# Kernel tuning notes

Hardware: AMD Instinct MI355X
Metric: run time of the kernel (lower is better)

Reference implementation:

```python
import jax, jax.numpy as jnp
import numpy as np

LENGTH = 4000
N_PAD = 4096  # smallest power of 2 >= LENGTH


def _hadamard(n: int) -> jnp.ndarray:
    """Sylvester-construction Hadamard matrix (matches scipy.linalg.hadamard)."""
    H = np.array([[1.0]], dtype=np.float32)
    while H.shape[0] < n:
        H = np.block([[H, H], [H, -H]])
    return jnp.asarray(H, dtype=jnp.float32)


def setup_inputs() -> dict:
    key = jax.random.key(0)
    k1, k2, k3, k4 = jax.random.split(key, 4)
    x = jax.random.normal(k1, (8, 64, LENGTH), dtype=jnp.float32)          # [B, Cin, L]
    W = jax.random.normal(k2, (4, 64, 64), dtype=jnp.float32) * 0.1       # [P, Cout, Cin] (1x1 conv, no bias)
    T = jax.random.uniform(k3, (4, N_PAD), dtype=jnp.float32) / 10.0      # per-pod soft thresholds
    v = jax.random.uniform(k4, (4, N_PAD), dtype=jnp.float32)             # per-pod spectral scale
    return {"x": x, "W": W, "T": T, "v": v}


def reference(x, W, T, v):
    H = _hadamard(N_PAD)                                                  # [n, n], symmetric
    # zero-pad to power of two
    f0 = jnp.pad(x, ((0, 0), (0, 0), (0, N_PAD - LENGTH)))                # [B, Cin, n]
    # forward WHT along last axis: u @ H
    f1 = f0 @ H                                                           # [B, Cin, n]
    # per-pod: v_i * f1 -> 1x1 conv -> soft-threshold
    z = v[:, None, None, :] * f1[None]                                    # [P, B, Cin, n]
    c = jnp.einsum('poi,pbin->pbon', W, z)                                # [P, B, Cout, n]
    st = jnp.sign(c) * jax.nn.relu(jnp.abs(c) - jnp.abs(T)[:, None, None, :])
    f6 = st.sum(axis=0)                                                   # [B, Cout, n]
    # inverse WHT: u @ H / n, then crop
    y = (f6 @ H) * (1.0 / N_PAD)
    y = y[..., :LENGTH]
    return y + x  # residual
```

## Files before the change

### kernel.cpp

```cpp
#include <hip/hip_runtime.h>
#include <hip/hip_bf16.h>

#define LENGTH 4000
#define NPAD   4096
#define NB     8
#define CH     64
#define NP     4
#define NT2    32
#define BSTR   72

using ushort8 = __attribute__((ext_vector_type(8))) unsigned short;
using short8v = __attribute__((ext_vector_type(8))) short;
using f32x4   = __attribute__((ext_vector_type(4))) float;

__device__ __forceinline__ unsigned short f2bu(float f) {
    __hip_bfloat16 h = __float2bfloat16(f);
    return __builtin_bit_cast(unsigned short, h);
}
__device__ __forceinline__ float bu2f(unsigned short u) {
    __hip_bfloat16 h = __builtin_bit_cast(__hip_bfloat16, u);
    return __bfloat162float(h);
}

__device__ __forceinline__ void fwht8(float v[8]) {
    #pragma unroll
    for (int h = 1; h < 8; h <<= 1)
        #pragma unroll
        for (int j = 0; j < 8; j += 2 * h)
            #pragma unroll
            for (int k = j; k < j + h; ++k) {
                float a = v[k], b = v[k + h];
                v[k] = a + b; v[k + h] = a - b;
            }
}

#define LADR(n) ((((n) >> 3) * 9) + ((n) & 7))
#define LDSZ 4608


__global__ __launch_bounds__(512) void k_fwht_fwd(const float* __restrict__ x,
                                                  unsigned short* __restrict__ f1t,
                                                  const float* __restrict__ W,
                                                  unsigned short* __restrict__ Wb) {
    __shared__ float ldsA[LDSZ];
    __shared__ float ldsB[LDSZ];
    const int row = blockIdx.x;
    const int t = threadIdx.x;

    if (row < NP * CH && t < CH)
        Wb[row * CH + t] = f2bu(W[row * CH + t]);

    float v[8];
    if (t < 500) {
        const float* xr = x + (size_t)row * LENGTH + t * 8;
        float4 a = *(const float4*)xr, b = *(const float4*)(xr + 4);
        v[0]=a.x; v[1]=a.y; v[2]=a.z; v[3]=a.w;
        v[4]=b.x; v[5]=b.y; v[6]=b.z; v[7]=b.w;
    } else {
        #pragma unroll
        for (int j = 0; j < 8; ++j) v[j] = 0.f;
    }
    fwht8(v);

    #pragma unroll
    for (int j = 0; j < 8; ++j) ldsA[LADR(t * 8 + j)] = v[j];
    __syncthreads();
    const int s1 = (t >> 3) * 64 + (t & 7);
    #pragma unroll
    for (int j = 0; j < 8; ++j) v[j] = ldsA[LADR(s1 + j * 8)];
    fwht8(v);

    #pragma unroll
    for (int j = 0; j < 8; ++j) ldsB[LADR(s1 + j * 8)] = v[j];
    __syncthreads();
    const int s2 = (t >> 6) * 512 + ((t >> 3) & 7) * 8 + (t & 7);
    #pragma unroll
    for (int j = 0; j < 8; ++j) v[j] = ldsB[LADR(s2 + j * 64)];
    fwht8(v);

    #pragma unroll
    for (int j = 0; j < 8; ++j) ldsA[LADR(s2 + j * 64)] = v[j];
    __syncthreads();
    #pragma unroll
    for (int j = 0; j < 8; ++j) v[j] = ldsA[LADR(j * 512 + t)];
    fwht8(v);

    const int b = row >> 6, i = row & 63;
    unsigned short* fb = f1t + ((size_t)b * 128 * 64 + (size_t)i) * 32;
    #pragma unroll
    for (int j = 0; j < 8; ++j) {
        const int n = j * 512 + t;
        fb[(size_t)(n >> 5) * (64 * 32) + (n & 31)] = f2bu(v[j]);
    }
}

__global__ __launch_bounds__(256) void k_mix(const unsigned short* __restrict__ f1t,
                                             const unsigned short* __restrict__ Wb,
                                             const float* __restrict__ T,
                                             const float* __restrict__ v,
                                             unsigned short* __restrict__ f6b) {
    __shared__ unsigned short sBt[NT2 * BSTR];
    const int bid = blockIdx.x;
    const int nchunk = bid & 127;
    const int b = bid >> 7;
    const int nbase = nchunk * NT2;
    const int t = threadIdx.x;
    const int lane = t & 63;
    const int w = t >> 6;
    const int l15 = lane & 15, lq = lane >> 4;

    {
        const unsigned short* src =
            f1t + (size_t)(b * 128 + nchunk) * (64 * 32) + t * 8;
        ushort8 r = *(const ushort8*)src;
        const int i = t >> 2, n0 = (t & 3) * 8;
        #pragma unroll
        for (int j = 0; j < 8; ++j)
            sBt[(n0 + j) * BSTR + i] = r[j];
    }

    short8v afrag[NP][2];
    #pragma unroll
    for (int p = 0; p < NP; ++p)
        #pragma unroll
        for (int ks = 0; ks < 2; ++ks)
            afrag[p][ks] = *(const short8v*)(Wb +
                (size_t)(p * 64 + w * 16 + l15) * CH + ks * 32 + lq * 8);

    float vp_[2][NP], tp_[2][NP];
    #pragma unroll
    for (int nt = 0; nt < 2; ++nt) {
        const int n = nbase + nt * 16 + l15;
        #pragma unroll
        for (int p = 0; p < NP; ++p) {
            vp_[nt][p] = v[(size_t)p * NPAD + n];
            tp_[nt][p] = fabsf(T[(size_t)p * NPAD + n]);
        }
    }

    __syncthreads();

    short8v bfrag[2][2];
    #pragma unroll
    for (int nt = 0; nt < 2; ++nt)
        #pragma unroll
        for (int ks = 0; ks < 2; ++ks)
            bfrag[nt][ks] = *(const short8v*)(
                &sBt[(nt * 16 + l15) * BSTR + ks * 32 + lq * 8]);

    f32x4 acc[NP][2];
    #pragma unroll
    for (int p = 0; p < NP; ++p)
        #pragma unroll
        for (int nt = 0; nt < 2; ++nt) {
            acc[p][nt] = (f32x4){0.f, 0.f, 0.f, 0.f};
            #pragma unroll
            for (int ks = 0; ks < 2; ++ks)
                acc[p][nt] = __builtin_amdgcn_mfma_f32_16x16x32_bf16(
                    afrag[p][ks], bfrag[nt][ks], acc[p][nt], 0, 0, 0);
        }

    #pragma unroll
    for (int nt = 0; nt < 2; ++nt) {
        const int n = nbase + nt * 16 + l15;
        float outv[4] = {0.f, 0.f, 0.f, 0.f};
        #pragma unroll
        for (int p = 0; p < NP; ++p) {
            #pragma unroll
            for (int r = 0; r < 4; ++r) {
                float c = vp_[nt][p] * acc[p][nt][r];
                float a = fabsf(c) - tp_[nt][p];
                outv[r] += (a > 0.f) ? copysignf(a, c) : 0.f;
            }
        }
        #pragma unroll
        for (int r = 0; r < 4; ++r) {
            const int o = w * 16 + lq * 4 + r;
            f6b[(size_t)(b * CH + o) * NPAD + n] = f2bu(outv[r]);
        }
    }
}

__global__ __launch_bounds__(512) void k_fwht_inv(const unsigned short* __restrict__ f6b,
                                                  const float* __restrict__ x,
                                                  float* __restrict__ out) {
    __shared__ float ldsA[LDSZ];
    __shared__ float ldsB[LDSZ];
    const int row = blockIdx.x;
    const int t = threadIdx.x;

    float v[8];
    {
        const unsigned short* fr = f6b + (size_t)row * NPAD + t * 8;
        ushort8 r = *(const ushort8*)fr;
        #pragma unroll
        for (int j = 0; j < 8; ++j) v[j] = bu2f(r[j]);
    }
    fwht8(v);

    #pragma unroll
    for (int j = 0; j < 8; ++j) ldsA[LADR(t * 8 + j)] = v[j];
    __syncthreads();
    const int s1 = (t >> 3) * 64 + (t & 7);
    #pragma unroll
    for (int j = 0; j < 8; ++j) v[j] = ldsA[LADR(s1 + j * 8)];
    fwht8(v);

    #pragma unroll
    for (int j = 0; j < 8; ++j) ldsB[LADR(s1 + j * 8)] = v[j];
    __syncthreads();
    const int s2 = (t >> 6) * 512 + ((t >> 3) & 7) * 8 + (t & 7);
    #pragma unroll
    for (int j = 0; j < 8; ++j) v[j] = ldsB[LADR(s2 + j * 64)];
    fwht8(v);

    #pragma unroll
    for (int j = 0; j < 8; ++j) ldsA[LADR(s2 + j * 64)] = v[j];
    __syncthreads();
    #pragma unroll
    for (int j = 0; j < 8; ++j) v[j] = ldsA[LADR(j * 512 + t)];
    fwht8(v);

    const float scale = 1.f / NPAD;
    const float* xr = x + (size_t)row * LENGTH;
    float* orow = out + (size_t)row * LENGTH;
    #pragma unroll
    for (int j = 0; j < 8; ++j) {
        const int n = j * 512 + t;
        if (n < LENGTH) orow[n] = v[j] * scale + xr[n];
    }
}

extern "C" void kernel_launch(void* const* d_in, const int* in_sizes, int n_in,
                              void* d_out, int out_size, void* d_ws, size_t ws_size,
                              hipStream_t stream) {
    (void)in_sizes; (void)n_in; (void)out_size; (void)ws_size;
    const float* x = (const float*)d_in[0];
    const float* W = (const float*)d_in[1];
    const float* T = (const float*)d_in[2];
    const float* v = (const float*)d_in[3];
    float* out = (float*)d_out;
    unsigned short* f1t = (unsigned short*)d_ws;
    unsigned short* f6b = f1t + (size_t)NB * CH * NPAD;
    unsigned short* Wb  = f6b + (size_t)NB * CH * NPAD;

    k_fwht_fwd<<<NB * CH, 512, 0, stream>>>(x, f1t, W, Wb);
    k_mix<<<NB * (NPAD / NT2), 256, 0, stream>>>(f1t, Wb, T, v, f6b);
    k_fwht_inv<<<NB * CH, 512, 0, stream>>>(f6b, x, out);
}
```

Baseline: 22.88 us.

## Compute forward and inverse WHT as two 64x64 Hadamard MFMA matmuls

Replaces the four-stage radix-8 butterfly WHT, which ran in fp32 in LDS, with a factorisation of the 4096-point transform as H64 x X x H64. Each row is reshaped to 64x64 bf16 in LDS and multiplied by Hadamard fragments generated on the fly with sign-flip bit patterns, using bf16 MFMA. This cuts block size to 256 threads, removes two sync stages and halves LDS traffic. In exchange, the input and the intermediate are rounded to bf16, which lowers accuracy.

New measurement: 23.52 us. +2.8%, slower.

```diff
diff --git a/kernel.cpp b/kernel.cpp
--- a/kernel.cpp
+++ b/kernel.cpp
@@ -8,89 +8,119 @@
 #define NP     4
 #define NT2    32
 #define BSTR   72
+#define HST    72
 
 using ushort8 = __attribute__((ext_vector_type(8))) unsigned short;
+using ushort4v = __attribute__((ext_vector_type(4))) unsigned short;
 using short8v = __attribute__((ext_vector_type(8))) short;
 using f32x4   = __attribute__((ext_vector_type(4))) float;
+using uint4v  = __attribute__((ext_vector_type(4))) unsigned int;
 
 __device__ __forceinline__ unsigned short f2bu(float f) {
     __hip_bfloat16 h = __float2bfloat16(f);
     return __builtin_bit_cast(unsigned short, h);
 }
-__device__ __forceinline__ float bu2f(unsigned short u) {
-    __hip_bfloat16 h = __builtin_bit_cast(__hip_bfloat16, u);
-    return __bfloat162float(h);
-}
-
-__device__ __forceinline__ void fwht8(float v[8]) {
-    #pragma unroll
-    for (int h = 1; h < 8; h <<= 1)
-        #pragma unroll
-        for (int j = 0; j < 8; j += 2 * h)
-            #pragma unroll
-            for (int k = j; k < j + h; ++k) {
-                float a = v[k], b = v[k + h];
-                v[k] = a + b; v[k + h] = a - b;
-            }
-}
-
-#define LADR(n) ((((n) >> 3) * 9) + ((n) & 7))
-#define LDSZ 4608
-
-
-__global__ __launch_bounds__(512) void k_fwht_fwd(const float* __restrict__ x,
+
+__device__ __forceinline__ short8v hfrag(const unsigned pat[4], int j, int k0) {
+    const unsigned flip = (__popc(j & k0) & 1) ? 0x80008000u : 0u;
+    uint4v r;
+    r[0] = pat[0] ^ flip; r[1] = pat[1] ^ flip;
+    r[2] = pat[2] ^ flip; r[3] = pat[3] ^ flip;
+    return __builtin_bit_cast(short8v, r);
+}
+
+__device__ __forceinline__ void mkpat(unsigned pat[4], int l15) {
+    const int jl = l15 & 7;
+    #pragma unroll
+    for (int d = 0; d < 4; ++d) {
+        unsigned lo = (__popc((2 * d) & jl) & 1) ? 0xBF80u : 0x3F80u;
+        unsigned hi = (__popc((2 * d + 1) & jl) & 1) ? 0xBF80u : 0x3F80u;
+        pat[d] = lo | (hi << 16);
+    }
+}
+
+__global__ __launch_bounds__(256) void k_fwht_fwd(const float* __restrict__ x,
                                                   unsigned short* __restrict__ f1t,
                                                   const float* __restrict__ W,
                                                   unsigned short* __restrict__ Wb) {
-    __shared__ float ldsA[LDSZ];
-    __shared__ float ldsB[LDSZ];
+    __shared__ unsigned short sX[64 * HST];
+    __shared__ unsigned short sT[64 * HST];
     const int row = blockIdx.x;
     const int t = threadIdx.x;
+    const int b = row >> 6, i = row & 63;
+    const int lane = t & 63, w = t >> 6;
+    const int l15 = lane & 15, lq = lane >> 4;
 
     if (row < NP * CH && t < CH)
         Wb[row * CH + t] = f2bu(W[row * CH + t]);
 
-    float v[8];
-    if (t < 500) {
-        const float* xr = x + (size_t)row * LENGTH + t * 8;
-        float4 a = *(const float4*)xr, b = *(const float4*)(xr + 4);
-        v[0]=a.x; v[1]=a.y; v[2]=a.z; v[3]=a.w;
-        v[4]=b.x; v[5]=b.y; v[6]=b.z; v[7]=b.w;
-    } else {
-        #pragma unroll
-        for (int j = 0; j < 8; ++j) v[j] = 0.f;
-    }
-    fwht8(v);
-
-    #pragma unroll
-    for (int j = 0; j < 8; ++j) ldsA[LADR(t * 8 + j)] = v[j];
-    __syncthreads();
-    const int s1 = (t >> 3) * 64 + (t & 7);
-    #pragma unroll
-    for (int j = 0; j < 8; ++j) v[j] = ldsA[LADR(s1 + j * 8)];
-    fwht8(v);
-
-    #pragma unroll
-    for (int j = 0; j < 8; ++j) ldsB[LADR(s1 + j * 8)] = v[j];
-    __syncthreads();
-    const int s2 = (t >> 6) * 512 + ((t >> 3) & 7) * 8 + (t & 7);
-    #pragma unroll
-    for (int j = 0; j < 8; ++j) v[j] = ldsB[LADR(s2 + j * 64)];
-    fwht8(v);
-
-    #pragma unroll
-    for (int j = 0; j < 8; ++j) ldsA[LADR(s2 + j * 64)] = v[j];
-    __syncthreads();
-    #pragma unroll
-    for (int j = 0; j < 8; ++j) v[j] = ldsA[LADR(j * 512 + t)];
-    fwht8(v);
-
-    const int b = row >> 6, i = row & 63;
-    unsigned short* fb = f1t + ((size_t)b * 128 * 64 + (size_t)i) * 32;
-    #pragma unroll
-    for (int j = 0; j < 8; ++j) {
-        const int n = j * 512 + t;
-        fb[(size_t)(n >> 5) * (64 * 32) + (n & 31)] = f2bu(v[j]);
+    {
+        unsigned short e16[16];
+        if (t < 250) {
+            const float* xr = x + (size_t)row * LENGTH + t * 16;
+            #pragma unroll
+            for (int q = 0; q < 4; ++q) {
+                float4 lv = *(const float4*)(xr + q * 4);
+                e16[q * 4 + 0] = f2bu(lv.x); e16[q * 4 + 1] = f2bu(lv.y);
+                e16[q * 4 + 2] = f2bu(lv.z); e16[q * 4 + 3] = f2bu(lv.w);
+            }
+        } else {
+            #pragma unroll
+            for (int q = 0; q < 16; ++q) e16[q] = 0;
+        }
+        const int a = t >> 2, c0 = (t & 3) * 16;
+        *(ushort8*)&sX[a * HST + c0]     = *(ushort8*)&e16[0];
+        *(ushort8*)&sX[a * HST + c0 + 8] = *(ushort8*)&e16[8];
+    }
+
+    unsigned pat[4];
+    mkpat(pat, l15);
+    __syncthreads();
+
+    f32x4 acc[4];
+    #pragma unroll
+    for (int nt = 0; nt < 4; ++nt) acc[nt] = (f32x4){0.f, 0.f, 0.f, 0.f};
+    #pragma unroll
+    for (int ks = 0; ks < 2; ++ks) {
+        const int k0 = ks * 32 + lq * 8;
+        short8v af = *(const short8v*)&sX[(w * 16 + l15) * HST + k0];
+        #pragma unroll
+        for (int nt = 0; nt < 4; ++nt)
+            acc[nt] = __builtin_amdgcn_mfma_f32_16x16x32_bf16(
+                af, hfrag(pat, nt * 16 + l15, k0), acc[nt], 0, 0, 0);
+    }
+    #pragma unroll
+    for (int nt = 0; nt < 4; ++nt) {
+        ushort4v u;
+        u[0] = f2bu(acc[nt][0]); u[1] = f2bu(acc[nt][1]);
+        u[2] = f2bu(acc[nt][2]); u[3] = f2bu(acc[nt][3]);
+        *(ushort4v*)&sT[(nt * 16 + l15) * HST + w * 16 + lq * 4] = u;
+    }
+    __syncthreads();
+
+    f32x4 acc2[4];
+    #pragma unroll
+    for (int nt = 0; nt < 4; ++nt) acc2[nt] = (f32x4){0.f, 0.f, 0.f, 0.f};
+    #pragma unroll
+    for (int ks = 0; ks < 2; ++ks) {
+        const int k0 = ks * 32 + lq * 8;
+        short8v af = hfrag(pat, w * 16 + l15, k0);
+        #pragma unroll
+        for (int nt = 0; nt < 4; ++nt) {
+            short8v bf = *(const short8v*)&sT[(nt * 16 + l15) * HST + k0];
+            acc2[nt] = __builtin_amdgcn_mfma_f32_16x16x32_bf16(
+                af, bf, acc2[nt], 0, 0, 0);
+        }
+    }
+    #pragma unroll
+    for (int nt = 0; nt < 4; ++nt) {
+        const int nl = (nt & 1) * 16 + l15;
+        #pragma unroll
+        for (int r = 0; r < 4; ++r) {
+            const int ap = w * 16 + lq * 4 + r;
+            f1t[((size_t)(b * 128 + ap * 2 + (nt >> 1)) * 64 + i) * 32 + nl] =
+                f2bu(acc2[nt][r]);
+        }
     }
 }
 
@@ -181,53 +211,77 @@
     }
 }
 
-__global__ __launch_bounds__(512) void k_fwht_inv(const unsigned short* __restrict__ f6b,
+__global__ __launch_bounds__(256) void k_fwht_inv(const unsigned short* __restrict__ f6b,
                                                   const float* __restrict__ x,
                                                   float* __restrict__ out) {
-    __shared__ float ldsA[LDSZ];
-    __shared__ float ldsB[LDSZ];
+    __shared__ unsigned short sM[64 * HST];
+    __shared__ unsigned short sT[64 * HST];
     const int row = blockIdx.x;
     const int t = threadIdx.x;
-
-    float v[8];
+    const int lane = t & 63, w = t >> 6;
+    const int l15 = lane & 15, lq = lane >> 4;
+
     {
-        const unsigned short* fr = f6b + (size_t)row * NPAD + t * 8;
-        ushort8 r = *(const ushort8*)fr;
-        #pragma unroll
-        for (int j = 0; j < 8; ++j) v[j] = bu2f(r[j]);
-    }
-    fwht8(v);
-
-    #pragma unroll
-    for (int j = 0; j < 8; ++j) ldsA[LADR(t * 8 + j)] = v[j];
-    __syncthreads();
-    const int s1 = (t >> 3) * 64 + (t & 7);
-    #pragma unroll
-    for (int j = 0; j < 8; ++j) v[j] = ldsA[LADR(s1 + j * 8)];
-    fwht8(v);
-
-    #pragma unroll
-    for (int j = 0; j < 8; ++j) ldsB[LADR(s1 + j * 8)] = v[j];
-    __syncthreads();
-    const int s2 = (t >> 6) * 512 + ((t >> 3) & 7) * 8 + (t & 7);
-    #pragma unroll
-    for (int j = 0; j < 8; ++j) v[j] = ldsB[LADR(s2 + j * 64)];
-    fwht8(v);
-
-    #pragma unroll
-    for (int j = 0; j < 8; ++j) ldsA[LADR(s2 + j * 64)] = v[j];
-    __syncthreads();
-    #pragma unroll
-    for (int j = 0; j < 8; ++j) v[j] = ldsA[LADR(j * 512 + t)];
-    fwht8(v);
+        const unsigned short* fr = f6b + (size_t)row * NPAD + t * 16;
+        ushort8 r0 = *(const ushort8*)fr;
+        ushort8 r1 = *(const ushort8*)(fr + 8);
+        const int ap = t >> 2, c0 = (t & 3) * 16;
+        *(ushort8*)&sM[ap * HST + c0]     = r0;
+        *(ushort8*)&sM[ap * HST + c0 + 8] = r1;
+    }
+
+    unsigned pat[4];
+    mkpat(pat, l15);
+    __syncthreads();
+
+    f32x4 acc[4];
+    #pragma unroll
+    for (int nt = 0; nt < 4; ++nt) acc[nt] = (f32x4){0.f, 0.f, 0.f, 0.f};
+    #pragma unroll
+    for (int ks = 0; ks < 2; ++ks) {
+        const int k0 = ks * 32 + lq * 8;
+        short8v af = *(const short8v*)&sM[(w * 16 + l15) * HST + k0];
+        #pragma unroll
+        for (int nt = 0; nt < 4; ++nt)
+            acc[nt] = __builtin_amdgcn_mfma_f32_16x16x32_bf16(
+                af, hfrag(pat, nt * 16 + l15, k0), acc[nt], 0, 0, 0);
+    }
+    #pragma unroll
+    for (int nt = 0; nt < 4; ++nt) {
+        ushort4v u;
+        u[0] = f2bu(acc[nt][0]); u[1] = f2bu(acc[nt][1]);
+        u[2] = f2bu(acc[nt][2]); u[3] = f2bu(acc[nt][3]);
+        *(ushort4v*)&sT[(nt * 16 + l15) * HST + w * 16 + lq * 4] = u;
+    }
+    __syncthreads();
+
+    f32x4 acc2[4];
+    #pragma unroll
+    for (int nt = 0; nt < 4; ++nt) acc2[nt] = (f32x4){0.f, 0.f, 0.f, 0.f};
+    #pragma unroll
+    for (int ks = 0; ks < 2; ++ks) {
+        const int k0 = ks * 32 + lq * 8;
+        short8v af = hfrag(pat, w * 16 + l15, k0);
+        #pragma unroll
+        for (int nt = 0; nt < 4; ++nt) {
+            short8v bf = *(const short8v*)&sT[(nt * 16 + l15) * HST + k0];
+            acc2[nt] = __builtin_amdgcn_mfma_f32_16x16x32_bf16(
+                af, bf, acc2[nt], 0, 0, 0);
+        }
+    }
 
     const float scale = 1.f / NPAD;
     const float* xr = x + (size_t)row * LENGTH;
     float* orow = out + (size_t)row * LENGTH;
     #pragma unroll
-    for (int j = 0; j < 8; ++j) {
-        const int n = j * 512 + t;
-        if (n < LENGTH) orow[n] = v[j] * scale + xr[n];
+    for (int nt = 0; nt < 4; ++nt) {
+        const int c = nt * 16 + l15;
+        #pragma unroll
+        for (int r = 0; r < 4; ++r) {
+            const int a = w * 16 + lq * 4 + r;
+            const int n = a * 64 + c;
+            if (n < LENGTH) orow[n] = acc2[nt][r] * scale + xr[n];
+        }
     }
 }
 
@@ -244,7 +298,7 @@
     unsigned short* f6b = f1t + (size_t)NB * CH * NPAD;
     unsigned short* Wb  = f6b + (size_t)NB * CH * NPAD;
 
-    k_fwht_fwd<<<NB * CH, 512, 0, stream>>>(x, f1t, W, Wb);
+    k_fwht_fwd<<<NB * CH, 256, 0, stream>>>(x, f1t, W, Wb);
     k_mix<<<NB * (NPAD / NT2), 256, 0, stream>>>(f1t, Wb, T, v, f6b);
-    k_fwht_inv<<<NB * CH, 512, 0, stream>>>(f6b, x, out);
-}
+    k_fwht_inv<<<NB * CH, 256, 0, stream>>>(f6b, x, out);
+}
```
